# Kernel tuning notes

Measured on AMD Instinct MI355X. Metric: run time of the kernel, lower is better.

Reference implementation:

```python
import jax, jax.numpy as jnp
import numpy as np

N_NODES = 100000
N_EDGES = 1600000
IN_F = 128
HID = 128
N_ACT = 32
N_GRAPHS = 256


def setup_inputs() -> dict:
    key = jax.random.key(0)
    ks = jax.random.split(key, 8)
    x = jax.random.normal(ks[0], (N_NODES, IN_F), dtype=jnp.float32)
    edge_index = jax.random.randint(ks[1], (2, N_EDGES), 0, N_NODES, dtype=jnp.int64 if jax.config.read('jax_enable_x64') else jnp.int32)
    batch = jnp.sort(jax.random.randint(ks[2], (N_NODES,), 0, N_GRAPHS))
    def glorot(k, shape):
        fan_in = shape[0]
        return jax.random.normal(k, shape, dtype=jnp.float32) / jnp.sqrt(jnp.float32(fan_in))
    return {
        'x': x,
        'edge_index': edge_index,
        'batch': batch,
        'W1': glorot(ks[3], (IN_F, HID)), 'b1': jnp.zeros((HID,), jnp.float32),
        'W2': glorot(ks[4], (HID, HID)), 'b2': jnp.zeros((HID,), jnp.float32),
        'Wl1': glorot(ks[5], (HID, HID)), 'bl1': jnp.zeros((HID,), jnp.float32),
        'Wl2': glorot(ks[6], (HID, N_ACT)), 'bl2': jnp.zeros((N_ACT,), jnp.float32),
    }


def gcn_conv(x, src, dst, W, b, n_nodes):
    """PyG GCNConv: add self-loops, sym-normalize by deg^{-1/2} (deg counted at dst)."""
    h = x @ W  # [N, F_out]
    # degree including self-loop (computed on destination/col, per gcn_norm)
    deg = jax.ops.segment_sum(jnp.ones((src.shape[0],), h.dtype), dst,
                              num_segments=n_nodes) + 1.0
    dinv = jax.lax.rsqrt(deg)  # deg >= 1, no inf handling needed
    norm = dinv[src] * dinv[dst]  # [E]
    agg = jax.ops.segment_sum(norm[:, None] * h[src], dst, num_segments=n_nodes)
    # self-loop contribution: dinv[i]^2 * h[i]
    return agg + (dinv * dinv)[:, None] * h + b


def global_mean_pool(x, batch, num_graphs):
    s = jax.ops.segment_sum(x, batch, num_segments=num_graphs)
    cnt = jax.ops.segment_sum(jnp.ones((x.shape[0],), x.dtype), batch,
                              num_segments=num_graphs)
    return s / jnp.maximum(cnt, 1.0)[:, None]


def reference(x, edge_index, batch, W1, b1, W2, b2, Wl1, bl1, Wl2, bl2):
    src, dst = edge_index[0], edge_index[1]
    n = x.shape[0]
    h = jax.nn.relu(gcn_conv(x, src, dst, W1, b1, n))
    h = jax.nn.relu(gcn_conv(h, src, dst, W2, b2, n))
    g = global_mean_pool(h, batch, N_GRAPHS)  # [G, HID]
    g = jax.nn.relu(g @ Wl1 + bl1)
    return g @ Wl2 + bl2  # [G, N_ACT]
```

## Files before the change

### kernel.cpp

```cpp
#include <hip/hip_runtime.h>
#include <hip/hip_bf16.h>

#define N_NODES 100000
#define N_EDGES 1600000
#define NFEAT   128
#define NGRAPH  256
#define NACT    32
#define ECAP    64
#define OVF_CAP 8192

#define BUCK_SHIFT 9
#define BUCK_NODES 512
#define NBUCK ((N_NODES + BUCK_NODES - 1) / BUCK_NODES)
#define SEGCAP 10240
#define CHUNK 4096
#define NBLK1 ((N_EDGES + CHUNK - 1) / CHUNK)
#define BIN_NODES 128
#define NBLK2 ((N_NODES + BIN_NODES - 1) / BIN_NODES)
#define GB ((N_NODES + 63) / 64)
#define WTBLK (2 * NFEAT * NFEAT / 256)
#define LDSROW 136

typedef __attribute__((ext_vector_type(8))) short bf16x8;
typedef __attribute__((ext_vector_type(4))) float f32x4;

__device__ inline unsigned short f2bf(float f) {
  __hip_bfloat16 b = __float2bfloat16(f);
  return *reinterpret_cast<unsigned short*>(&b);
}
__device__ inline float2 bfu2f(unsigned u) {
  __hip_bfloat162 t = *reinterpret_cast<__hip_bfloat162*>(&u);
  return __bfloat1622float2(t);
}

__global__ __launch_bounds__(256) void edgepart_wt_kernel(const int* __restrict__ src,
                                                          const int* __restrict__ dst,
                                                          int* __restrict__ bucket_cursor,
                                                          int2* __restrict__ seg,
                                                          int* __restrict__ cnt,
                                                          int* __restrict__ ovf_cnt,
                                                          int* __restrict__ ovf,
                                                          const float* __restrict__ W1,
                                                          const float* __restrict__ W2,
                                                          unsigned short* __restrict__ Wt1,
                                                          unsigned short* __restrict__ Wt2) {
  __shared__ int2 stage[CHUNK];
  __shared__ int hist[NBUCK], offs[NBUCK], cursor[NBUCK], gbase[NBUCK];
  __shared__ int sc[256];
  int tid = threadIdx.x;

  if (blockIdx.x >= NBLK1) {
    int i = (blockIdx.x - NBLK1) * 256 + tid;
    int which = i >> 14;
    int idx = i & 16383;
    int n = idx >> 7, k = idx & 127;
    if (which == 0) Wt1[n * NFEAT + k] = f2bf(W1[k * NFEAT + n]);
    else            Wt2[n * NFEAT + k] = f2bf(W2[k * NFEAT + n]);
    return;
  }

  int e0 = blockIdx.x * CHUNK;
  int m = N_EDGES - e0; if (m > CHUNK) m = CHUNK;

  for (int i = tid; i < NBUCK; i += 256) hist[i] = 0;
  __syncthreads();

  for (int i = tid; i < m; i += 256)
    atomicAdd(&hist[dst[e0 + i] >> BUCK_SHIFT], 1);
  __syncthreads();

  sc[tid] = (tid < NBUCK) ? hist[tid] : 0;
  __syncthreads();
  for (int ofs = 1; ofs < 256; ofs <<= 1) {
    int t = (tid >= ofs) ? sc[tid - ofs] : 0;
    __syncthreads();
    sc[tid] += t;
    __syncthreads();
  }
  if (tid < NBUCK) {
    int o = tid ? sc[tid - 1] : 0;
    offs[tid] = o;
    cursor[tid] = o;
    gbase[tid] = hist[tid] ? atomicAdd(&bucket_cursor[tid], hist[tid]) : 0;
  }
  __syncthreads();

  for (int i = tid; i < m; i += 256) {
    int2 p = make_int2(src[e0 + i], dst[e0 + i]);
    int pos = atomicAdd(&cursor[p.y >> BUCK_SHIFT], 1);
    stage[pos] = p;
  }
  __syncthreads();

  for (int i = tid; i < m; i += 256) {
    int2 p = stage[i];
    int bd = p.y >> BUCK_SHIFT;
    int gpos = gbase[bd] + (i - offs[bd]);
    if (gpos < SEGCAP) {
      seg[(size_t)bd * SEGCAP + gpos] = p;
    } else {
      atomicAdd(&cnt[p.y], 1);
      int o = atomicAdd(ovf_cnt, 1);
      if (o < OVF_CAP) { ovf[2 * o] = p.x; ovf[2 * o + 1] = p.y; }
    }
  }
}

__global__ __launch_bounds__(256) void binbuild_gemm_kernel(const int2* __restrict__ seg,
                                                            const int* __restrict__ bucket_cursor,
                                                            int* __restrict__ cnt,
                                                            float* __restrict__ dinv,
                                                            int* __restrict__ elist,
                                                            int* __restrict__ ovf_cnt,
                                                            int* __restrict__ ovf,
                                                            const float* __restrict__ x,
                                                            const unsigned short* __restrict__ Wt,
                                                            unsigned short* __restrict__ C) {
  __shared__ int lcnt[BIN_NODES];
  __shared__ int lel[BIN_NODES * ECAP];
  int tid = threadIdx.x;

  if (blockIdx.x >= NBLK2) {
    int bid = blockIdx.x - NBLK2;
    int wave = tid >> 6, lane = tid & 63;
    int q = lane >> 4, r = lane & 15;
    int m0 = bid * 64 + wave * 16;
    int arow = m0 + r; if (arow > N_NODES - 1) arow = N_NODES - 1;
    const float* Arow = x + (size_t)arow * NFEAT;

    f32x4 acc[8];
    #pragma unroll
    for (int t = 0; t < 8; ++t) acc[t] = (f32x4){0.f, 0.f, 0.f, 0.f};

    #pragma unroll
    for (int s = 0; s < 4; ++s) {
      int k0 = s * 32 + q * 8;
      float4 a0 = *(const float4*)(Arow + k0);
      float4 a1 = *(const float4*)(Arow + k0 + 4);
      bf16x8 xf;
      xf[0] = (short)f2bf(a0.x); xf[1] = (short)f2bf(a0.y);
      xf[2] = (short)f2bf(a0.z); xf[3] = (short)f2bf(a0.w);
      xf[4] = (short)f2bf(a1.x); xf[5] = (short)f2bf(a1.y);
      xf[6] = (short)f2bf(a1.z); xf[7] = (short)f2bf(a1.w);
      #pragma unroll
      for (int t = 0; t < 8; ++t) {
        bf16x8 wf = *(const bf16x8*)(Wt + (size_t)(t * 16 + r) * NFEAT + k0);
        acc[t] = __builtin_amdgcn_mfma_f32_16x16x32_bf16(wf, xf, acc[t], 0, 0, 0);
      }
    }
    int node = m0 + r;
    if (node < N_NODES) {
      uint2* Crow = (uint2*)(C + (size_t)node * NFEAT);
      #pragma unroll
      for (int t = 0; t < 8; ++t) {
        uint2 v;
        v.x = ((unsigned)f2bf(acc[t][1]) << 16) | f2bf(acc[t][0]);
        v.y = ((unsigned)f2bf(acc[t][3]) << 16) | f2bf(acc[t][2]);
        Crow[t * 4 + q] = v;
      }
    }
    return;
  }

  int n0 = blockIdx.x * BIN_NODES;
  int pb = n0 >> BUCK_SHIFT;
  if (tid < BIN_NODES) lcnt[tid] = 0;
  __syncthreads();
  int m = bucket_cursor[pb]; if (m > SEGCAP) m = SEGCAP;
  const int2* s = seg + (size_t)pb * SEGCAP;
  for (int e = tid; e < m; e += 256) {
    int2 p = s[e];
    unsigned ln = (unsigned)(p.y - n0);
    if (ln < (unsigned)BIN_NODES) {
      int pos = atomicAdd(&lcnt[ln], 1);
      if (pos < ECAP) {
        lel[(ln << 6) + pos] = p.x;
      } else {
        int o = atomicAdd(ovf_cnt, 1);
        if (o < OVF_CAP) { ovf[2 * o] = p.x; ovf[2 * o + 1] = p.y; }
      }
    }
  }
  __syncthreads();
  if (tid < BIN_NODES) {
    int n = n0 + tid;
    if (n < N_NODES) {
      int tot = cnt[n] + lcnt[tid];
      cnt[n] = tot;
      dinv[n] = rsqrtf((float)tot + 1.0f);
    }
  }
  int4* gel = (int4*)(elist + (size_t)n0 * ECAP);
  const int4* lel4 = (const int4*)lel;
  for (int i = tid; i < BIN_NODES * ECAP / 4; i += 256) gel[i] = lel4[i];
}

__global__ __launch_bounds__(512) void agg_gemm_kernel(const uint2* __restrict__ h2,
                                                       const int* __restrict__ elist,
                                                       const int* __restrict__ cnt,
                                                       const float* __restrict__ dinv,
                                                       const float* __restrict__ bias,
                                                       const int* __restrict__ ovf_cnt,
                                                       const int* __restrict__ ovf,
                                                       const unsigned short* __restrict__ Wt2,
                                                       unsigned short* __restrict__ H2) {
  __shared__ __align__(16) unsigned short hloc[16 * LDSROW];
  int tid = threadIdx.x;
  int lane = tid & 63;
  int lw = tid >> 6;
  int hl = lane & 31;
  int n0 = blockIdx.x * 16;
  int nloc = lw * 2 + (lane >> 5);
  int n = n0 + nloc;

  float dn = dinv[n];
  int c = cnt[n]; c = (c > ECAP) ? ECAP : c;
  const int* el = elist + (size_t)n * ECAP;

  int   s0 = (hl < c)      ? el[hl]      : n;
  float w0 = (hl < c)      ? dinv[s0] * dn : 0.f;
  int   s1 = (hl + 32 < c) ? el[hl + 32] : n;
  float w1 = (hl + 32 < c) ? dinv[s1] * dn : 0.f;

  int cA = __shfl(c, 0), cB = __shfl(c, 32);
  int cmax = cA > cB ? cA : cB;

  uint2 hv = h2[(size_t)n * 32 + hl];
  float2 vlo = bfu2f(hv.x), vhi = bfu2f(hv.y);
  float sw = dn * dn;
  float a0 = sw * vlo.x, a1 = sw * vlo.y, a2 = sw * vhi.x, a3 = sw * vhi.y;

  int e1 = cmax < 32 ? cmax : 32;
  e1 = (e1 + 7) & ~7;
  for (int j = 0; j < e1; j += 8) {
    uint2 pv[8]; float w[8];
    #pragma unroll
    for (int u = 0; u < 8; ++u) {
      int s = __shfl(s0, j + u, 32);
      w[u] = __shfl(w0, j + u, 32);
      pv[u] = h2[(size_t)s * 32 + hl];
    }
    #pragma unroll
    for (int u = 0; u < 8; ++u) {
      float2 lo = bfu2f(pv[u].x), hi = bfu2f(pv[u].y);
      a0 = fmaf(w[u], lo.x, a0); a1 = fmaf(w[u], lo.y, a1);
      a2 = fmaf(w[u], hi.x, a2); a3 = fmaf(w[u], hi.y, a3);
    }
  }
  if (cmax > 32) {
    int e2 = ((cmax - 32) + 7) & ~7;
    for (int j = 0; j < e2; j += 8) {
      uint2 pv[8]; float w[8];
      #pragma unroll
      for (int u = 0; u < 8; ++u) {
        int s = __shfl(s1, j + u, 32);
        w[u] = __shfl(w1, j + u, 32);
        pv[u] = h2[(size_t)s * 32 + hl];
      }
      #pragma unroll
      for (int u = 0; u < 8; ++u) {
        float2 lo = bfu2f(pv[u].x), hi = bfu2f(pv[u].y);
        a0 = fmaf(w[u], lo.x, a0); a1 = fmaf(w[u], lo.y, a1);
        a2 = fmaf(w[u], hi.x, a2); a3 = fmaf(w[u], hi.y, a3);
      }
    }
  }

  int m = *ovf_cnt; if (m > OVF_CAP) m = OVF_CAP;
  for (int p = 0; p < m; ++p) {
    int s = ovf[2 * p], d = ovf[2 * p + 1];
    if (d == n) {
      float w = dinv[s] * dn;
      uint2 pv = h2[(size_t)s * 32 + hl];
      float2 lo = bfu2f(pv.x), hi = bfu2f(pv.y);
      a0 = fmaf(w, lo.x, a0); a1 = fmaf(w, lo.y, a1);
      a2 = fmaf(w, hi.x, a2); a3 = fmaf(w, hi.y, a3);
    }
  }

  float4 b4 = ((const float4*)bias)[hl];
  uint2 v;
  v.x = ((unsigned)f2bf(fmaxf(a1 + b4.y, 0.f)) << 16) | f2bf(fmaxf(a0 + b4.x, 0.f));
  v.y = ((unsigned)f2bf(fmaxf(a3 + b4.w, 0.f)) << 16) | f2bf(fmaxf(a2 + b4.z, 0.f));
  *(uint2*)(&hloc[nloc * LDSROW + hl * 4]) = v;
  __syncthreads();

  int q = lane >> 4, r = lane & 15;
  int node = n0 + r;
  float dvr = dinv[node];
  f32x4 acc = (f32x4){0.f, 0.f, 0.f, 0.f};
  #pragma unroll
  for (int s = 0; s < 4; ++s) {
    int k0 = s * 32 + q * 8;
    bf16x8 xf = *(const bf16x8*)(&hloc[r * LDSROW + k0]);
    bf16x8 wf = *(const bf16x8*)(Wt2 + (size_t)(lw * 16 + r) * NFEAT + k0);
    acc = __builtin_amdgcn_mfma_f32_16x16x32_bf16(wf, xf, acc, 0, 0, 0);
  }
  uint2* Crow = (uint2*)(H2 + (size_t)node * NFEAT);
  uint2 o;
  o.x = ((unsigned)f2bf(dvr * acc[1]) << 16) | f2bf(dvr * acc[0]);
  o.y = ((unsigned)f2bf(dvr * acc[3]) << 16) | f2bf(dvr * acc[2]);
  Crow[lw * 4 + q] = o;
}

__global__ __launch_bounds__(256) void agg_pool_kernel(const uint2* __restrict__ h2,
                                                       const int* __restrict__ elist,
                                                       const int* __restrict__ cnt,
                                                       const float* __restrict__ dinv,
                                                       const float* __restrict__ bias,
                                                       const int* __restrict__ ovf_cnt,
                                                       const int* __restrict__ ovf,
                                                       const int* __restrict__ batch,
                                                       float* __restrict__ gsum) {
  __shared__ float lds[8][NFEAT];
  int tid = threadIdx.x;
  int wid = (blockIdx.x * 256 + tid) >> 6;
  int lane = tid & 63;
  int hl = lane & 31;
  int n = wid * 2 + (lane >> 5);
  int n0 = blockIdx.x * 8;

  float dn = dinv[n];
  int c = cnt[n]; c = (c > ECAP) ? ECAP : c;
  const int* el = elist + (size_t)n * ECAP;

  int s0 = (hl < c)      ? el[hl]      : n;
  int s1 = (hl + 32 < c) ? el[hl + 32] : n;

  int cA = __shfl(c, 0), cB = __shfl(c, 32);
  int cmax = cA > cB ? cA : cB;

  uint2 hv = h2[(size_t)n * 32 + hl];
  float2 vlo = bfu2f(hv.x), vhi = bfu2f(hv.y);
  float a0 = vlo.x, a1 = vlo.y, a2 = vhi.x, a3 = vhi.y;

  int e1 = cmax < 32 ? cmax : 32;
  e1 = (e1 + 7) & ~7;
  for (int j = 0; j < e1; j += 8) {
    uint2 pv[8];
    #pragma unroll
    for (int u = 0; u < 8; ++u) {
      int s = __shfl(s0, j + u, 32);
      pv[u] = h2[(size_t)s * 32 + hl];
    }
    #pragma unroll
    for (int u = 0; u < 8; ++u) {
      if (j + u < c) {
        float2 lo = bfu2f(pv[u].x), hi = bfu2f(pv[u].y);
        a0 += lo.x; a1 += lo.y; a2 += hi.x; a3 += hi.y;
      }
    }
  }
  if (cmax > 32) {
    int e2 = 32 + (((cmax - 32) + 7) & ~7);
    for (int j = 32; j < e2; j += 8) {
      uint2 pv[8];
      #pragma unroll
      for (int u = 0; u < 8; ++u) {
        int s = __shfl(s1, j - 32 + u, 32);
        pv[u] = h2[(size_t)s * 32 + hl];
      }
      #pragma unroll
      for (int u = 0; u < 8; ++u) {
        if (j + u < c) {
          float2 lo = bfu2f(pv[u].x), hi = bfu2f(pv[u].y);
          a0 += lo.x; a1 += lo.y; a2 += hi.x; a3 += hi.y;
        }
      }
    }
  }

  int m = *ovf_cnt; if (m > OVF_CAP) m = OVF_CAP;
  for (int p = 0; p < m; ++p) {
    int s = ovf[2 * p], d = ovf[2 * p + 1];
    if (d == n) {
      uint2 pv = h2[(size_t)s * 32 + hl];
      float2 lo = bfu2f(pv.x), hi = bfu2f(pv.y);
      a0 += lo.x; a1 += lo.y; a2 += hi.x; a3 += hi.y;
    }
  }

  float4 b4 = ((const float4*)bias)[hl];
  int nloc = n - n0;
  lds[nloc][hl * 4 + 0] = fmaxf(fmaf(dn, a0, b4.x), 0.f);
  lds[nloc][hl * 4 + 1] = fmaxf(fmaf(dn, a1, b4.y), 0.f);
  lds[nloc][hl * 4 + 2] = fmaxf(fmaf(dn, a2, b4.z), 0.f);
  lds[nloc][hl * 4 + 3] = fmaxf(fmaf(dn, a3, b4.w), 0.f);
  __syncthreads();

  if (tid < NFEAT) {
    float sum = 0.f;
    int cur = batch[n0];
    #pragma unroll
    for (int i = 0; i < 8; ++i) {
      int b = batch[n0 + i];
      if (b != cur) {
        atomicAdd(&gsum[cur * NFEAT + tid], sum);
        sum = 0.f; cur = b;
      }
      sum += lds[i][tid];
    }
    atomicAdd(&gsum[cur * NFEAT + tid], sum);
  }
}

__global__ __launch_bounds__(128) void mlp_kernel(const float* __restrict__ gsum,
                                                  const int* __restrict__ batch,
                                                  const float* __restrict__ Wl1,
                                                  const float* __restrict__ bl1,
                                                  const float* __restrict__ Wl2,
                                                  const float* __restrict__ bl2,
                                                  float* __restrict__ out) {
  __shared__ float gr[NFEAT];
  __shared__ float t1[NFEAT];
  __shared__ float sinv;
  int g = blockIdx.x, t = threadIdx.x;
  if (t == 0) {
    int lo = 0, hi = N_NODES;
    while (lo < hi) { int mid = (lo + hi) >> 1; if (batch[mid] < g) lo = mid + 1; else hi = mid; }
    int lo2 = lo, hi2 = N_NODES;
    while (lo2 < hi2) { int mid = (lo2 + hi2) >> 1; if (batch[mid] < g + 1) lo2 = mid + 1; else hi2 = mid; }
    sinv = 1.0f / fmaxf((float)(lo2 - lo), 1.0f);
  }
  __syncthreads();
  gr[t] = gsum[g * NFEAT + t] * sinv;
  __syncthreads();
  float acc = bl1[t];
  for (int k = 0; k < NFEAT; ++k) acc = fmaf(gr[k], Wl1[k * NFEAT + t], acc);
  t1[t] = fmaxf(acc, 0.f);
  __syncthreads();
  if (t < NACT) {
    float a2 = bl2[t];
    for (int k = 0; k < NFEAT; ++k) a2 = fmaf(t1[k], Wl2[k * NACT + t], a2);
    out[g * NACT + t] = a2;
  }
}

extern "C" void kernel_launch(void* const* d_in, const int* in_sizes, int n_in,
                              void* d_out, int out_size, void* d_ws, size_t ws_size,
                              hipStream_t stream) {
  const float* x    = (const float*)d_in[0];
  const int*   ei   = (const int*)d_in[1];
  const int*   batch= (const int*)d_in[2];
  const float* W1   = (const float*)d_in[3];
  const float* b1   = (const float*)d_in[4];
  const float* W2   = (const float*)d_in[5];
  const float* b2   = (const float*)d_in[6];
  const float* Wl1  = (const float*)d_in[7];
  const float* bl1  = (const float*)d_in[8];
  const float* Wl2  = (const float*)d_in[9];
  const float* bl2  = (const float*)d_in[10];
  float* out = (float*)d_out;

  const int* srcp = ei;
  const int* dstp = ei + N_EDGES;

  char* base = (char*)d_ws;
  size_t off = 0;
  auto alloc = [&](size_t bytes) -> void* {
    void* p = base + off;
    off += (bytes + 511) & ~(size_t)511;
    return p;
  };
  int*   cnt     = (int*)alloc((size_t)N_NODES * 4);
  int*   ovfc    = (int*)alloc(4);
  float* gsum    = (float*)alloc((size_t)NGRAPH * NFEAT * 4);
  int*   bucket_cursor = (int*)alloc((size_t)NBUCK * 4);
  size_t zspan   = off;
  float* dinv    = (float*)alloc((size_t)N_NODES * 4);
  int*   elist   = (int*)alloc((size_t)NBLK2 * BIN_NODES * ECAP * 4);
  int*   ovf     = (int*)alloc((size_t)OVF_CAP * 2 * 4);
  int2*  seg     = (int2*)alloc((size_t)NBUCK * SEGCAP * 8);
  unsigned short* Wt1 = (unsigned short*)alloc((size_t)NFEAT * NFEAT * 2);
  unsigned short* Wt2 = (unsigned short*)alloc((size_t)NFEAT * NFEAT * 2);
  unsigned short* H1 = (unsigned short*)alloc((size_t)N_NODES * NFEAT * 2);
  unsigned short* H2 = (unsigned short*)alloc((size_t)N_NODES * NFEAT * 2);

  hipMemsetAsync(d_ws, 0, zspan, stream);

  const int AB = (N_NODES + 7) / 8;
  const int FB = N_NODES / 16;

  edgepart_wt_kernel<<<NBLK1 + WTBLK, 256, 0, stream>>>(
      srcp, dstp, bucket_cursor, seg, cnt, ovfc, ovf, W1, W2, Wt1, Wt2);
  binbuild_gemm_kernel<<<NBLK2 + GB, 256, 0, stream>>>(
      seg, bucket_cursor, cnt, dinv, elist, ovfc, ovf, x, Wt1, H1);
  agg_gemm_kernel<<<FB, 512, 0, stream>>>((const uint2*)H1, elist, cnt, dinv, b1,
                                          ovfc, ovf, Wt2, H2);
  agg_pool_kernel<<<AB, 256, 0, stream>>>((const uint2*)H2, elist, cnt, dinv, b2,
                                          ovfc, ovf, batch, gsum);
  mlp_kernel<<<NGRAPH, 128, 0, stream>>>(gsum, batch, Wl1, bl1, Wl2, bl2, out);
}
```

Baseline: 317.5 us.

## Split agg_pool feature dimension across two blocks with 4-byte gathers

The second aggregation+pool kernel now launches twice as many blocks, each handling half the 128 features (64 bf16 values) for 8 nodes, so every 32-lane group gathers 4-byte words instead of 8-byte ones. Loop bounds are now per-node counts rather than the max across two nodes, and the gather unroll goes from 8 to 16 to keep more loads in flight. This raises parallelism and memory-level concurrency on the latency-bound gather. In exchange, edge-list reads, overflow scans and atomics to gsum are duplicated per half, and each gather now moves narrower transactions.

```diff
diff --git a/kernel.cpp b/kernel.cpp
--- a/kernel.cpp
+++ b/kernel.cpp
@@ -303,7 +303,7 @@
   Crow[lw * 4 + q] = o;
 }
 
-__global__ __launch_bounds__(256) void agg_pool_kernel(const uint2* __restrict__ h2,
+__global__ __launch_bounds__(256) void agg_pool_kernel(const unsigned* __restrict__ hu,
                                                        const int* __restrict__ elist,
                                                        const int* __restrict__ cnt,
                                                        const float* __restrict__ dinv,
@@ -312,13 +312,14 @@
                                                        const int* __restrict__ ovf,
                                                        const int* __restrict__ batch,
                                                        float* __restrict__ gsum) {
-  __shared__ float lds[8][NFEAT];
+  __shared__ float lds[8][64];
   int tid = threadIdx.x;
-  int wid = (blockIdx.x * 256 + tid) >> 6;
-  int lane = tid & 63;
-  int hl = lane & 31;
-  int n = wid * 2 + (lane >> 5);
-  int n0 = blockIdx.x * 8;
+  int half = blockIdx.x & 1;
+  int nb   = blockIdx.x >> 1;
+  int nloc = tid >> 5;
+  int hl   = tid & 31;
+  int n0 = nb * 8;
+  int n = n0 + nloc;
 
   float dn = dinv[n];
   int c = cnt[n]; c = (c > ECAP) ? ECAP : c;
@@ -327,44 +328,42 @@
   int s0 = (hl < c)      ? el[hl]      : n;
   int s1 = (hl + 32 < c) ? el[hl + 32] : n;
 
-  int cA = __shfl(c, 0), cB = __shfl(c, 32);
-  int cmax = cA > cB ? cA : cB;
-
-  uint2 hv = h2[(size_t)n * 32 + hl];
-  float2 vlo = bfu2f(hv.x), vhi = bfu2f(hv.y);
-  float a0 = vlo.x, a1 = vlo.y, a2 = vhi.x, a3 = vhi.y;
-
-  int e1 = cmax < 32 ? cmax : 32;
-  e1 = (e1 + 7) & ~7;
-  for (int j = 0; j < e1; j += 8) {
-    uint2 pv[8];
-    #pragma unroll
-    for (int u = 0; u < 8; ++u) {
+  int base = half * 32 + hl;
+  unsigned hv = hu[(size_t)n * 64 + base];
+  float2 v = bfu2f(hv);
+  float a0 = v.x, a1 = v.y;
+
+  int e1 = c < 32 ? c : 32;
+  e1 = (e1 + 15) & ~15;
+  for (int j = 0; j < e1; j += 16) {
+    unsigned pv[16];
+    #pragma unroll
+    for (int u = 0; u < 16; ++u) {
       int s = __shfl(s0, j + u, 32);
-      pv[u] = h2[(size_t)s * 32 + hl];
-    }
-    #pragma unroll
-    for (int u = 0; u < 8; ++u) {
+      pv[u] = hu[(size_t)s * 64 + base];
+    }
+    #pragma unroll
+    for (int u = 0; u < 16; ++u) {
       if (j + u < c) {
-        float2 lo = bfu2f(pv[u].x), hi = bfu2f(pv[u].y);
-        a0 += lo.x; a1 += lo.y; a2 += hi.x; a3 += hi.y;
-      }
-    }
-  }
-  if (cmax > 32) {
-    int e2 = 32 + (((cmax - 32) + 7) & ~7);
-    for (int j = 32; j < e2; j += 8) {
-      uint2 pv[8];
-      #pragma unroll
-      for (int u = 0; u < 8; ++u) {
-        int s = __shfl(s1, j - 32 + u, 32);
-        pv[u] = h2[(size_t)s * 32 + hl];
-      }
-      #pragma unroll
-      for (int u = 0; u < 8; ++u) {
-        if (j + u < c) {
-          float2 lo = bfu2f(pv[u].x), hi = bfu2f(pv[u].y);
-          a0 += lo.x; a1 += lo.y; a2 += hi.x; a3 += hi.y;
+        float2 f = bfu2f(pv[u]);
+        a0 += f.x; a1 += f.y;
+      }
+    }
+  }
+  if (c > 32) {
+    int e2 = ((c - 32) + 15) & ~15;
+    for (int j = 0; j < e2; j += 16) {
+      unsigned pv[16];
+      #pragma unroll
+      for (int u = 0; u < 16; ++u) {
+        int s = __shfl(s1, j + u, 32);
+        pv[u] = hu[(size_t)s * 64 + base];
+      }
+      #pragma unroll
+      for (int u = 0; u < 16; ++u) {
+        if (32 + j + u < c) {
+          float2 f = bfu2f(pv[u]);
+          a0 += f.x; a1 += f.y;
         }
       }
     }
@@ -374,33 +373,29 @@
   for (int p = 0; p < m; ++p) {
     int s = ovf[2 * p], d = ovf[2 * p + 1];
     if (d == n) {
-      uint2 pv = h2[(size_t)s * 32 + hl];
-      float2 lo = bfu2f(pv.x), hi = bfu2f(pv.y);
-      a0 += lo.x; a1 += lo.y; a2 += hi.x; a3 += hi.y;
-    }
-  }
-
-  float4 b4 = ((const float4*)bias)[hl];
-  int nloc = n - n0;
-  lds[nloc][hl * 4 + 0] = fmaxf(fmaf(dn, a0, b4.x), 0.f);
-  lds[nloc][hl * 4 + 1] = fmaxf(fmaf(dn, a1, b4.y), 0.f);
-  lds[nloc][hl * 4 + 2] = fmaxf(fmaf(dn, a2, b4.z), 0.f);
-  lds[nloc][hl * 4 + 3] = fmaxf(fmaf(dn, a3, b4.w), 0.f);
-  __syncthreads();
-
-  if (tid < NFEAT) {
+      float2 f = bfu2f(hu[(size_t)s * 64 + base]);
+      a0 += f.x; a1 += f.y;
+    }
+  }
+
+  float2 b2v = ((const float2*)bias)[half * 32 + hl];
+  lds[nloc][hl * 2 + 0] = fmaxf(fmaf(dn, a0, b2v.x), 0.f);
+  lds[nloc][hl * 2 + 1] = fmaxf(fmaf(dn, a1, b2v.y), 0.f);
+  __syncthreads();
+
+  if (tid < 64) {
     float sum = 0.f;
     int cur = batch[n0];
     #pragma unroll
     for (int i = 0; i < 8; ++i) {
       int b = batch[n0 + i];
       if (b != cur) {
-        atomicAdd(&gsum[cur * NFEAT + tid], sum);
+        atomicAdd(&gsum[cur * NFEAT + half * 64 + tid], sum);
         sum = 0.f; cur = b;
       }
       sum += lds[i][tid];
     }
-    atomicAdd(&gsum[cur * NFEAT + tid], sum);
+    atomicAdd(&gsum[cur * NFEAT + half * 64 + tid], sum);
   }
 }
 
@@ -478,7 +473,7 @@
 
   hipMemsetAsync(d_ws, 0, zspan, stream);
 
-  const int AB = (N_NODES + 7) / 8;
+  const int AB = (N_NODES / 8) * 2;
   const int FB = N_NODES / 16;
 
   edgepart_wt_kernel<<<NBLK1 + WTBLK, 256, 0, stream>>>(
@@ -487,7 +482,7 @@
       seg, bucket_cursor, cnt, dinv, elist, ovfc, ovf, x, Wt1, H1);
   agg_gemm_kernel<<<FB, 512, 0, stream>>>((const uint2*)H1, elist, cnt, dinv, b1,
                                           ovfc, ovf, Wt2, H2);
-  agg_pool_kernel<<<AB, 256, 0, stream>>>((const uint2*)H2, elist, cnt, dinv, b2,
+  agg_pool_kernel<<<AB, 256, 0, stream>>>((const unsigned*)H2, elist, cnt, dinv, b2,
                                           ovfc, ovf, batch, gsum);
   mlp_kernel<<<NGRAPH, 128, 0, stream>>>(gsum, batch, Wl1, bl1, Wl2, bl2, out);
 }
```

New measurement: 322.4 us. About the same (+1.5%).

## Move layer-1 GEMM into edge-partition kernel with per-block LDS weight transpose

Applied to the files above, without the earlier changes.

The x@W1 GEMM blocks move from the bin-build kernel into the first (edge-partition) kernel. Each GEMM block converts and transposes W1 into LDS itself, so the separate Wt1 global buffer is no longer needed. The intent is to balance work across the first two launches and overlap the dense GEMM with the edge bucketing. In exchange, every GEMM block redoes the 128x128 conversion, and the shared LDS union (about 36KB) may reduce occupancy for the edge-partition blocks.

```diff
diff --git a/kernel.cpp b/kernel.cpp
--- a/kernel.cpp
+++ b/kernel.cpp
@@ -15,10 +15,10 @@
 #define SEGCAP 10240
 #define CHUNK 4096
 #define NBLK1 ((N_EDGES + CHUNK - 1) / CHUNK)
+#define WT2BLK 64
 #define BIN_NODES 128
 #define NBLK2 ((N_NODES + BIN_NODES - 1) / BIN_NODES)
 #define GB ((N_NODES + 63) / 64)
-#define WTBLK (2 * NFEAT * NFEAT / 256)
 #define LDSROW 136
 
 typedef __attribute__((ext_vector_type(8))) short bf16x8;
@@ -33,31 +33,78 @@
   return __bfloat1622float2(t);
 }
 
-__global__ __launch_bounds__(256) void edgepart_wt_kernel(const int* __restrict__ src,
-                                                          const int* __restrict__ dst,
-                                                          int* __restrict__ bucket_cursor,
-                                                          int2* __restrict__ seg,
-                                                          int* __restrict__ cnt,
-                                                          int* __restrict__ ovf_cnt,
-                                                          int* __restrict__ ovf,
-                                                          const float* __restrict__ W1,
-                                                          const float* __restrict__ W2,
-                                                          unsigned short* __restrict__ Wt1,
-                                                          unsigned short* __restrict__ Wt2) {
-  __shared__ int2 stage[CHUNK];
-  __shared__ int hist[NBUCK], offs[NBUCK], cursor[NBUCK], gbase[NBUCK];
-  __shared__ int sc[256];
+__global__ __launch_bounds__(256) void edgepart_wt_gemm1_kernel(
+    const int* __restrict__ src, const int* __restrict__ dst,
+    int* __restrict__ bucket_cursor, int2* __restrict__ seg,
+    int* __restrict__ cnt, int* __restrict__ ovf_cnt, int* __restrict__ ovf,
+    const float* __restrict__ W1, const float* __restrict__ W2,
+    unsigned short* __restrict__ Wt2,
+    const float* __restrict__ x, unsigned short* __restrict__ C) {
+  __shared__ __align__(16) char smem[36928];
   int tid = threadIdx.x;
+
+  if (blockIdx.x >= NBLK1 + WT2BLK) {
+    unsigned short* wtile = (unsigned short*)smem;
+    for (int i = tid; i < NFEAT * NFEAT; i += 256) {
+      int k = i >> 7, n = i & 127;
+      wtile[n * LDSROW + k] = f2bf(W1[i]);
+    }
+    __syncthreads();
+
+    int bid = blockIdx.x - NBLK1 - WT2BLK;
+    int wave = tid >> 6, lane = tid & 63;
+    int q = lane >> 4, r = lane & 15;
+    int m0 = bid * 64 + wave * 16;
+    int arow = m0 + r; if (arow > N_NODES - 1) arow = N_NODES - 1;
+    const float* Arow = x + (size_t)arow * NFEAT;
+
+    f32x4 acc[8];
+    #pragma unroll
+    for (int t = 0; t < 8; ++t) acc[t] = (f32x4){0.f, 0.f, 0.f, 0.f};
+
+    #pragma unroll
+    for (int s = 0; s < 4; ++s) {
+      int k0 = s * 32 + q * 8;
+      float4 a0 = *(const float4*)(Arow + k0);
+      float4 a1 = *(const float4*)(Arow + k0 + 4);
+      bf16x8 xf;
+      xf[0] = (short)f2bf(a0.x); xf[1] = (short)f2bf(a0.y);
+      xf[2] = (short)f2bf(a0.z); xf[3] = (short)f2bf(a0.w);
+      xf[4] = (short)f2bf(a1.x); xf[5] = (short)f2bf(a1.y);
+      xf[6] = (short)f2bf(a1.z); xf[7] = (short)f2bf(a1.w);
+      #pragma unroll
+      for (int t = 0; t < 8; ++t) {
+        bf16x8 wf = *(const bf16x8*)(wtile + (size_t)(t * 16 + r) * LDSROW + k0);
+        acc[t] = __builtin_amdgcn_mfma_f32_16x16x32_bf16(wf, xf, acc[t], 0, 0, 0);
+      }
+    }
+    int node = m0 + r;
+    if (node < N_NODES) {
+      uint2* Crow = (uint2*)(C + (size_t)node * NFEAT);
+      #pragma unroll
+      for (int t = 0; t < 8; ++t) {
+        uint2 v;
+        v.x = ((unsigned)f2bf(acc[t][1]) << 16) | f2bf(acc[t][0]);
+        v.y = ((unsigned)f2bf(acc[t][3]) << 16) | f2bf(acc[t][2]);
+        Crow[t * 4 + q] = v;
+      }
+    }
+    return;
+  }
 
   if (blockIdx.x >= NBLK1) {
     int i = (blockIdx.x - NBLK1) * 256 + tid;
-    int which = i >> 14;
-    int idx = i & 16383;
-    int n = idx >> 7, k = idx & 127;
-    if (which == 0) Wt1[n * NFEAT + k] = f2bf(W1[k * NFEAT + n]);
-    else            Wt2[n * NFEAT + k] = f2bf(W2[k * NFEAT + n]);
+    int n = i >> 7, k = i & 127;
+    Wt2[n * NFEAT + k] = f2bf(W2[k * NFEAT + n]);
     return;
   }
+
+  int2* stage = (int2*)smem;
+  int* hist   = (int*)(smem + 32768);
+  int* offs   = hist + NBUCK;
+  int* cursor = offs + NBUCK;
+  int* gbase  = cursor + NBUCK;
+  int* sc     = gbase + NBUCK;
 
   int e0 = blockIdx.x * CHUNK;
   int m = N_EDGES - e0; if (m > CHUNK) m = CHUNK;
@@ -106,61 +153,16 @@
   }
 }
 
-__global__ __launch_bounds__(256) void binbuild_gemm_kernel(const int2* __restrict__ seg,
-                                                            const int* __restrict__ bucket_cursor,
-                                                            int* __restrict__ cnt,
-                                                            float* __restrict__ dinv,
-                                                            int* __restrict__ elist,
-                                                            int* __restrict__ ovf_cnt,
-                                                            int* __restrict__ ovf,
-                                                            const float* __restrict__ x,
-                                                            const unsigned short* __restrict__ Wt,
-                                                            unsigned short* __restrict__ C) {
+__global__ __launch_bounds__(256) void binbuild_kernel(const int2* __restrict__ seg,
+                                                       const int* __restrict__ bucket_cursor,
+                                                       int* __restrict__ cnt,
+                                                       float* __restrict__ dinv,
+                                                       int* __restrict__ elist,
+                                                       int* __restrict__ ovf_cnt,
+                                                       int* __restrict__ ovf) {
   __shared__ int lcnt[BIN_NODES];
   __shared__ int lel[BIN_NODES * ECAP];
   int tid = threadIdx.x;
-
-  if (blockIdx.x >= NBLK2) {
-    int bid = blockIdx.x - NBLK2;
-    int wave = tid >> 6, lane = tid & 63;
-    int q = lane >> 4, r = lane & 15;
-    int m0 = bid * 64 + wave * 16;
-    int arow = m0 + r; if (arow > N_NODES - 1) arow = N_NODES - 1;
-    const float* Arow = x + (size_t)arow * NFEAT;
-
-    f32x4 acc[8];
-    #pragma unroll
-    for (int t = 0; t < 8; ++t) acc[t] = (f32x4){0.f, 0.f, 0.f, 0.f};
-
-    #pragma unroll
-    for (int s = 0; s < 4; ++s) {
-      int k0 = s * 32 + q * 8;
-      float4 a0 = *(const float4*)(Arow + k0);
-      float4 a1 = *(const float4*)(Arow + k0 + 4);
-      bf16x8 xf;
-      xf[0] = (short)f2bf(a0.x); xf[1] = (short)f2bf(a0.y);
-      xf[2] = (short)f2bf(a0.z); xf[3] = (short)f2bf(a0.w);
-      xf[4] = (short)f2bf(a1.x); xf[5] = (short)f2bf(a1.y);
-      xf[6] = (short)f2bf(a1.z); xf[7] = (short)f2bf(a1.w);
-      #pragma unroll
-      for (int t = 0; t < 8; ++t) {
-        bf16x8 wf = *(const bf16x8*)(Wt + (size_t)(t * 16 + r) * NFEAT + k0);
-        acc[t] = __builtin_amdgcn_mfma_f32_16x16x32_bf16(wf, xf, acc[t], 0, 0, 0);
-      }
-    }
-    int node = m0 + r;
-    if (node < N_NODES) {
-      uint2* Crow = (uint2*)(C + (size_t)node * NFEAT);
-      #pragma unroll
-      for (int t = 0; t < 8; ++t) {
-        uint2 v;
-        v.x = ((unsigned)f2bf(acc[t][1]) << 16) | f2bf(acc[t][0]);
-        v.y = ((unsigned)f2bf(acc[t][3]) << 16) | f2bf(acc[t][2]);
-        Crow[t * 4 + q] = v;
-      }
-    }
-    return;
-  }
 
   int n0 = blockIdx.x * BIN_NODES;
   int pb = n0 >> BUCK_SHIFT;
@@ -471,7 +473,6 @@
   int*   elist   = (int*)alloc((size_t)NBLK2 * BIN_NODES * ECAP * 4);
   int*   ovf     = (int*)alloc((size_t)OVF_CAP * 2 * 4);
   int2*  seg     = (int2*)alloc((size_t)NBUCK * SEGCAP * 8);
-  unsigned short* Wt1 = (unsigned short*)alloc((size_t)NFEAT * NFEAT * 2);
   unsigned short* Wt2 = (unsigned short*)alloc((size_t)NFEAT * NFEAT * 2);
   unsigned short* H1 = (unsigned short*)alloc((size_t)N_NODES * NFEAT * 2);
   unsigned short* H2 = (unsigned short*)alloc((size_t)N_NODES * NFEAT * 2);
@@ -481,10 +482,10 @@
   const int AB = (N_NODES + 7) / 8;
   const int FB = N_NODES / 16;
 
-  edgepart_wt_kernel<<<NBLK1 + WTBLK, 256, 0, stream>>>(
-      srcp, dstp, bucket_cursor, seg, cnt, ovfc, ovf, W1, W2, Wt1, Wt2);
-  binbuild_gemm_kernel<<<NBLK2 + GB, 256, 0, stream>>>(
-      seg, bucket_cursor, cnt, dinv, elist, ovfc, ovf, x, Wt1, H1);
+  edgepart_wt_gemm1_kernel<<<NBLK1 + WT2BLK + GB, 256, 0, stream>>>(
+      srcp, dstp, bucket_cursor, seg, cnt, ovfc, ovf, W1, W2, Wt2, x, H1);
+  binbuild_kernel<<<NBLK2, 256, 0, stream>>>(
+      seg, bucket_cursor, cnt, dinv, elist, ovfc, ovf);
   agg_gemm_kernel<<<FB, 512, 0, stream>>>((const uint2*)H1, elist, cnt, dinv, b1,
                                           ovfc, ovf, Wt2, H2);
   agg_pool_kernel<<<AB, 256, 0, stream>>>((const uint2*)H2, elist, cnt, dinv, b2,
```

Result: faster. 306.1 us (-3.6%).
